# Optimization experiments

Hardware: AMD Instinct MI355X
Metric: run time of the kernel (lower is better)

Reference implementation:

```python
import jax, jax.numpy as jnp
import numpy as np

N = 8192   # number of points (p) == number of reference points (r); must match for final bmm
D = 1024   # feature width of the Linear projections


def setup_inputs() -> dict:
    key = jax.random.key(0)
    ks = jax.random.split(key, 8)
    s = 1.0 / np.sqrt(D)
    return {
        "p": jax.random.normal(ks[0], (N, D), dtype=jnp.float32),
        "r": jax.random.normal(ks[1], (N, D), dtype=jnp.float32),
        "Wh": jax.random.uniform(ks[2], (D, D), jnp.float32, -s, s),
        "bh": jax.random.uniform(ks[3], (D,), jnp.float32, -s, s),
        "Wl": jax.random.uniform(ks[4], (D, D), jnp.float32, -s, s),
        "bl": jax.random.uniform(ks[5], (D,), jnp.float32, -s, s),
        "Wg": jax.random.uniform(ks[6], (D, D), jnp.float32, -s, s),
        "bg": jax.random.uniform(ks[7], (D,), jnp.float32, -s, s),
    }


def reference(p, r, Wh, bh, Wl, bl, Wg, bg):
    # Linear projections (torch Linear: x @ W.T + b)
    q = p @ Wh.T + bh          # [N, D]  M_h(p)
    k = r @ Wl.T + bl          # [N, D]  M_l(r)
    v = p @ Wg.T + bg          # [N, D]  M_g(p)
    scores = q @ k.T           # [N, N]  == bmm(q[None], k[None].transpose(1,2))[0]
    # torch softmax dim=1 on [1, N, N] normalizes over the QUERY axis -> axis=0 here
    attn = jax.nn.softmax(scores, axis=0)
    return p + attn @ v        # residual add
```

## Files before the change

### kernel.cpp

```cpp
#include <hip/hip_runtime.h>
#include <hip/hip_fp16.h>

typedef _Float16 f16;
typedef __attribute__((ext_vector_type(8))) _Float16 f16x8;
typedef __attribute__((ext_vector_type(4))) float f32x4;

#define NPTS 8192
#define DIM  1024
#define HL2E 0.721347520444482f
#define S2SHIFT 50.0f
#define TBUF (128 * 32)

__device__ __forceinline__ void glds16(const void* g, void* l) {
  __builtin_amdgcn_global_load_lds(
      (const __attribute__((address_space(1))) void*)g,
      (__attribute__((address_space(3))) void*)l, 16, 0, 0);
}


__global__ void cvt_f32_f16(const float* __restrict__ src, f16* __restrict__ dst, int n) {
  int i = (blockIdx.x * 256 + threadIdx.x) * 8;
  if (i >= n) return;
  const float4* s = (const float4*)(src + i);
  float4 a = s[0], b = s[1];
  f16x8 o;
  o[0] = (f16)a.x; o[1] = (f16)a.y; o[2] = (f16)a.z; o[3] = (f16)a.w;
  o[4] = (f16)b.x; o[5] = (f16)b.y; o[6] = (f16)b.z; o[7] = (f16)b.w;
  *(f16x8*)(dst + i) = o;
}

__global__ void zero_f32(float* __restrict__ p, int n) {
  int i = blockIdx.x * 256 + threadIdx.x;
  if (i < n) p[i] = 0.f;
}

__global__ void mk_scales(const float* __restrict__ colsum,
                          f16* __restrict__ ics2, f16* __restrict__ ics4) {
  int j = blockIdx.x * 256 + threadIdx.x;
  float r2 = rsqrtf(colsum[j]);
  ics2[j] = (f16)r2;
  ics4[j] = (f16)sqrtf(r2);
}

__global__ void vscale(f16* __restrict__ vt, const f16* __restrict__ ics2) {
  long i = ((long)blockIdx.x * 256 + threadIdx.x) * 8;
  f16x8 v = *(f16x8*)(vt + i);
  f16x8 s = *(const f16x8*)(ics2 + (i & (NPTS - 1)));
  *(f16x8*)(vt + i) = v * s;
}

__global__ void reduce_out(const float* __restrict__ p,
                           const float* __restrict__ pa,
                           const float* __restrict__ pb,
                           float* __restrict__ out) {
  long i = ((long)blockIdx.x * 256 + threadIdx.x) * 4;
  float4 a = *(const float4*)(p + i);
  float4 b = *(const float4*)(pa + i);
  float4 c = *(const float4*)(pb + i);
  a.x += b.x + c.x; a.y += b.y + c.y; a.z += b.z + c.z; a.w += b.w + c.w;
  *(float4*)(out + i) = a;
}

__global__ __launch_bounds__(256, 2)
void proj_fused(const f16* __restrict__ p_h, const f16* __restrict__ r_h,
                const f16* __restrict__ Wh, const f16* __restrict__ Wl,
                const f16* __restrict__ Wg,
                const float* __restrict__ bh, const float* __restrict__ bl,
                const float* __restrict__ bg,
                f16* __restrict__ q_h, f16* __restrict__ k_h,
                f16* __restrict__ vt_h) {
  __shared__ f16 sA[2 * TBUF];
  __shared__ f16 sB[2 * TBUF];
  const int sub = blockIdx.x >> 9;
  const int bl_ = blockIdx.x & 511;
  const long bi = (long)(bl_ & 63) * 128;
  const long bj = (long)(bl_ >> 6) * 128;
  const f16* A = (sub == 1) ? r_h : p_h;
  const f16* B = (sub == 0) ? Wh : (sub == 1) ? Wl : Wg;
  const float* bias = (sub == 0) ? bh : (sub == 1) ? bl : bg;

  const int t = threadIdx.x;
  const int w = t >> 6, l = t & 63;
  const int wm = (w >> 1) * 64, wn = (w & 1) * 64;
  const int lr = l & 15;
  const int fbase = lr * 32 + (((l >> 4) ^ ((lr >> 1) & 3)) * 8);
  const int grow = w * 16 + (l >> 2);
  const int gcol = ((l & 3) ^ ((l >> 3) & 3)) * 8;
  const f16* gA = A + (bi + grow) * (long)DIM + gcol;
  const f16* gB = B + (bj + grow) * (long)DIM + gcol;
  const int lw0 = (w * 16) * 32, lw1 = (64 + w * 16) * 32;

  glds16(gA, sA + lw0);
  glds16(gA + 64l * DIM, sA + lw1);
  glds16(gB, sB + lw0);
  glds16(gB + 64l * DIM, sB + lw1);
  gA += 32; gB += 32;

  f32x4 acc[4][4] = {};
  const int nk = DIM / 32;
  for (int k = 0; k < nk; k++) {
    const int cur = (k & 1) * TBUF, nxt = TBUF - cur;
    __syncthreads();
    if (k + 1 < nk) {
      glds16(gA, sA + nxt + lw0);
      glds16(gA + 64l * DIM, sA + nxt + lw1);
      glds16(gB, sB + nxt + lw0);
      glds16(gB + 64l * DIM, sB + nxt + lw1);
      gA += 32; gB += 32;
    }
    f16x8 af[4], bf[4];
#pragma unroll
    for (int mt = 0; mt < 4; mt++)
      af[mt] = *(const f16x8*)(sA + cur + (wm + mt * 16) * 32 + fbase);
#pragma unroll
    for (int nt = 0; nt < 4; nt++)
      bf[nt] = *(const f16x8*)(sB + cur + (wn + nt * 16) * 32 + fbase);
#pragma unroll
    for (int mt = 0; mt < 4; mt++)
#pragma unroll
      for (int nt = 0; nt < 4; nt++)
        acc[mt][nt] = __builtin_amdgcn_mfma_f32_16x16x32_f16(af[mt], bf[nt], acc[mt][nt], 0, 0, 0);
  }

  const int rbase = (l >> 4) * 4;
  f16* C = (sub == 0) ? q_h : (sub == 1) ? k_h : vt_h;
#pragma unroll
  for (int nt = 0; nt < 4; nt++) {
    const long col = bj + wn + nt * 16 + lr;
    const float bb = bias[col];
#pragma unroll
    for (int mt = 0; mt < 4; mt++) {
      const long row0 = bi + wm + mt * 16 + rbase;
      if (sub < 2) {
#pragma unroll
        for (int g = 0; g < 4; g++)
          C[(row0 + g) * DIM + col] = (f16)(acc[mt][nt][g] + bb);
      } else {
        union { unsigned long long u; f16 h[4]; } pk;
#pragma unroll
        for (int g = 0; g < 4; g++) pk.h[g] = (f16)(acc[mt][nt][g] + bb);
        *(unsigned long long*)(C + col * (long)NPTS + row0) = pk.u;
      }
    }
  }
}

__global__ __launch_bounds__(512, 2)
void gemm_qk(const f16* __restrict__ A, const f16* __restrict__ B,
             f16* __restrict__ S, float* __restrict__ colsum) {
  __shared__ f16 smem[4 * 16384];
  const int b = blockIdx.x;
  const int sx = b & 7;
  const int j = b >> 3;
  const long bi = (long)(j >> 2) * 256;
  const long bj = (long)(sx * 4 + (j & 3)) * 256;

  const int t = threadIdx.x;
  const int w = t >> 6, l = t & 63;
  const int wm = (w >> 2) * 128, wn = (w & 3) * 64;
  const int lr = l & 15;
  const int fbase = lr * 32 + (((l >> 4) ^ ((lr >> 1) & 3)) * 8);
  const int sro = t >> 2;
  const int scol = ((t & 3) ^ ((t >> 3) & 3)) * 8;
  const f16* gAs = A + (bi + sro) * (long)DIM + scol;
  const f16* gBs = B + (bj + sro) * (long)DIM + scol;
  const int ldst = w * 512;

#pragma unroll
  for (int tl = 0; tl < 3; ++tl) {
    f16* d = smem + tl * 16384;
    glds16(gAs + tl * 32,              d + ldst);
    glds16(gAs + tl * 32 + 128l * DIM, d + 4096 + ldst);
    glds16(gBs + tl * 32,              d + 8192 + ldst);
    glds16(gBs + tl * 32 + 128l * DIM, d + 12288 + ldst);
  }
  asm volatile("s_waitcnt vmcnt(8)" ::: "memory");
  __builtin_amdgcn_s_barrier();
  asm volatile("" ::: "memory");

  f32x4 acc[8][4] = {};
#pragma unroll 4
  for (int kt = 0; kt < 32; ++kt) {
    const f16* sa = smem + (kt & 3) * 16384;
    f16* d = smem + ((kt + 3) & 3) * 16384;
    const int ks = (kt + 3 < 32) ? (kt + 3) : 31;
    const f16* as_ = gAs + ks * 32;
    const f16* bs_ = gBs + ks * 32;
    f16x8 af[4], bf[4];

#pragma unroll
    for (int mt = 0; mt < 4; ++mt)
      af[mt] = *(const f16x8*)(sa + (wm + mt * 16) * 32 + fbase);
#pragma unroll
    for (int nt = 0; nt < 4; ++nt)
      bf[nt] = *(const f16x8*)(sa + 8192 + (wn + nt * 16) * 32 + fbase);
    glds16(as_,              d + ldst);
    glds16(as_ + 128l * DIM, d + 4096 + ldst);
#pragma unroll
    for (int mt = 0; mt < 4; ++mt)
#pragma unroll
      for (int nt = 0; nt < 4; ++nt)
        acc[mt][nt] = __builtin_amdgcn_mfma_f32_16x16x32_f16(af[mt], bf[nt], acc[mt][nt], 0, 0, 0);

#pragma unroll
    for (int mt = 0; mt < 4; ++mt)
      af[mt] = *(const f16x8*)(sa + (wm + 64 + mt * 16) * 32 + fbase);
    glds16(bs_,              d + 8192 + ldst);
    glds16(bs_ + 128l * DIM, d + 12288 + ldst);
#pragma unroll
    for (int mt = 0; mt < 4; ++mt)
#pragma unroll
      for (int nt = 0; nt < 4; ++nt)
        acc[4 + mt][nt] = __builtin_amdgcn_mfma_f32_16x16x32_f16(af[mt], bf[nt], acc[4 + mt][nt], 0, 0, 0);

    asm volatile("s_waitcnt vmcnt(8)" ::: "memory");
    __builtin_amdgcn_s_barrier();
    asm volatile("" ::: "memory");
  }

  const int rbase = (l >> 4) * 4;
  float csum[4] = {0.f, 0.f, 0.f, 0.f};
#pragma unroll
  for (int mt = 0; mt < 8; ++mt) {
#pragma unroll
    for (int g = 0; g < 4; ++g) {
      const long row = bi + wm + mt * 16 + rbase + g;
      f16* Srow = S + row * NPTS + bj + wn + lr;
#pragma unroll
      for (int nt = 0; nt < 4; ++nt) {
        float e = exp2f((acc[mt][nt][g] - S2SHIFT) * HL2E);
        e = fminf(e, 240.f);
        f16 eh = (f16)e;
        Srow[nt * 16] = eh;
        float ef = (float)eh;
        csum[nt] += ef * ef;
      }
    }
  }
#pragma unroll
  for (int nt = 0; nt < 4; ++nt) {
    float cs = csum[nt];
    cs += __shfl_xor(cs, 16);
    cs += __shfl_xor(cs, 32);
    if (l < 16) atomicAdd(colsum + (bj + wn + nt * 16 + lr), cs);
  }
}

__global__ __launch_bounds__(256, 2)
void gemm_pv(const f16* __restrict__ Sm, const f16* __restrict__ vt,
             const f16* __restrict__ ics4,
             float* __restrict__ part0, float* __restrict__ part1) {
  __shared__ f16 sA[2 * TBUF];
  __shared__ f16 sB[2 * TBUF];
  const int split = blockIdx.x >> 9;
  const int bl_ = blockIdx.x & 511;
  const long bi = (long)(bl_ & 63) * 128;
  const long bj = (long)(bl_ >> 6) * 128;
  const long koff = (long)split * (NPTS / 2);

  const int t = threadIdx.x;
  const int w = t >> 6, l = t & 63;
  const int wm = (w >> 1) * 64, wn = (w & 1) * 64;
  const int lr = l & 15;
  const int fbase = lr * 32 + (((l >> 4) ^ ((lr >> 1) & 3)) * 8);
  const int grow = w * 16 + (l >> 2);
  const int gcol = ((l & 3) ^ ((l >> 3) & 3)) * 8;
  const f16* gB = vt + (bj + grow) * (long)NPTS + koff + gcol;
  const int lw0 = (w * 16) * 32, lw1 = (64 + w * 16) * 32;

  const int sr = t >> 2, sc = (t & 3) * 8;
  const int ssw = ((t & 3) ^ ((t >> 3) & 3)) * 8;
  const f16* gAs = Sm + (bi + sr) * (long)NPTS + koff + sc;
  const f16* gIc = ics4 + koff + sc;
  f16x8 ra0, ra1, icv;

  const int nk = (NPTS / 2) / 32;

  ra0 = *(const f16x8*)gAs;
  ra1 = *(const f16x8*)(gAs + 64l * NPTS);
  icv = *(const f16x8*)gIc;
  {
    f16x8 t0 = ra0 * icv; t0 = t0 * t0;
    f16x8 t1 = ra1 * icv; t1 = t1 * t1;
    *(f16x8*)(sA + sr * 32 + ssw) = t0;
    *(f16x8*)(sA + (sr + 64) * 32 + ssw) = t1;
  }
  gAs += 32; gIc += 32;
  ra0 = *(const f16x8*)gAs;
  ra1 = *(const f16x8*)(gAs + 64l * NPTS);
  icv = *(const f16x8*)gIc;
  glds16(gB, sB + lw0);
  glds16(gB + 64l * NPTS, sB + lw1);
  gB += 32;

  f32x4 acc[4][4] = {};
  for (int k = 0; k < nk; k++) {
    const int cur = (k & 1) * TBUF, nxt = TBUF - cur;
    __syncthreads();
    if (k + 1 < nk) {
      f16x8 t0 = ra0 * icv; t0 = t0 * t0;
      f16x8 t1 = ra1 * icv; t1 = t1 * t1;
      *(f16x8*)(sA + nxt + sr * 32 + ssw) = t0;
      *(f16x8*)(sA + nxt + (sr + 64) * 32 + ssw) = t1;
      if (k + 2 < nk) {
        gAs += 32; gIc += 32;
        ra0 = *(const f16x8*)gAs;
        ra1 = *(const f16x8*)(gAs + 64l * NPTS);
        icv = *(const f16x8*)gIc;
      }
      glds16(gB, sB + nxt + lw0);
      glds16(gB + 64l * NPTS, sB + nxt + lw1);
      gB += 32;
    }
    f16x8 af[4], bf[4];
#pragma unroll
    for (int mt = 0; mt < 4; mt++)
      af[mt] = *(const f16x8*)(sA + cur + (wm + mt * 16) * 32 + fbase);
#pragma unroll
    for (int nt = 0; nt < 4; nt++)
      bf[nt] = *(const f16x8*)(sB + cur + (wn + nt * 16) * 32 + fbase);
#pragma unroll
    for (int mt = 0; mt < 4; mt++)
#pragma unroll
      for (int nt = 0; nt < 4; nt++)
        acc[mt][nt] = __builtin_amdgcn_mfma_f32_16x16x32_f16(af[mt], bf[nt], acc[mt][nt], 0, 0, 0);
  }

  float* part = split ? part1 : part0;
  const int rbase = (l >> 4) * 4;
#pragma unroll
  for (int nt = 0; nt < 4; nt++) {
    const long col = bj + wn + nt * 16 + lr;
#pragma unroll
    for (int mt = 0; mt < 4; mt++) {
      const long row0 = bi + wm + mt * 16 + rbase;
#pragma unroll
      for (int g = 0; g < 4; g++)
        part[(row0 + g) * DIM + col] = acc[mt][nt][g];
    }
  }
}

extern "C" void kernel_launch(void* const* d_in, const int* in_sizes, int n_in,
                              void* d_out, int out_size, void* d_ws, size_t ws_size,
                              hipStream_t stream) {
  const float* p  = (const float*)d_in[0];
  const float* r  = (const float*)d_in[1];
  const float* Wh = (const float*)d_in[2];
  const float* bh = (const float*)d_in[3];
  const float* Wl = (const float*)d_in[4];
  const float* bl = (const float*)d_in[5];
  const float* Wg = (const float*)d_in[6];
  const float* bg = (const float*)d_in[7];
  float* out = (float*)d_out;

  char* ws = (char*)d_ws;
  f16* q_h  = (f16*)(ws + (0ull  << 20));
  f16* k_h  = (f16*)(ws + (16ull << 20));
  f16* vt_h = (f16*)(ws + (32ull << 20));
  f16* p_h  = (f16*)(ws + (48ull << 20));
  f16* r_h  = (f16*)(ws + (64ull << 20));
  f16* wh_h = (f16*)(ws + (80ull << 20));
  f16* wl_h = (f16*)(ws + (82ull << 20));
  f16* wg_h = (f16*)(ws + (84ull << 20));
  f16* S    = (f16*)(ws + (96ull << 20));
  float* colsum = (float*)(ws + (224ull << 20));
  f16* ics2 = (f16*)(ws + (225ull << 20));
  f16* ics4 = (f16*)(ws + (226ull << 20));
  float* part0 = (float*)(ws + (0ull  << 20));
  float* part1 = (float*)(ws + (48ull << 20));

  const int nP = NPTS * DIM, nW = DIM * DIM;
  cvt_f32_f16<<<nP / 2048, 256, 0, stream>>>(p,  p_h,  nP);
  cvt_f32_f16<<<nP / 2048, 256, 0, stream>>>(r,  r_h,  nP);
  cvt_f32_f16<<<nW / 2048, 256, 0, stream>>>(Wh, wh_h, nW);
  cvt_f32_f16<<<nW / 2048, 256, 0, stream>>>(Wl, wl_h, nW);
  cvt_f32_f16<<<nW / 2048, 256, 0, stream>>>(Wg, wg_h, nW);
  zero_f32<<<NPTS / 256, 256, 0, stream>>>(colsum, NPTS);

  dim3 blk(256);
  proj_fused<<<1536, blk, 0, stream>>>(p_h, r_h, wh_h, wl_h, wg_h,
                                       bh, bl, bg, q_h, k_h, vt_h);
  gemm_qk<<<1024, dim3(512), 0, stream>>>(q_h, k_h, S, colsum);
  mk_scales<<<NPTS / 256, 256, 0, stream>>>(colsum, ics2, ics4);
  vscale<<<(NPTS / 8) * (DIM / 256), 256, 0, stream>>>(vt_h, ics2);
  gemm_pv<<<1024, blk, 0, stream>>>(S, vt_h, ics4, part0, part1);
  reduce_out<<<nP / 1024, 256, 0, stream>>>(p, part0, part1, out);
}
```

Measured before the change: 537.7 us.

## Restructure PV GEMM with 256x256 tiles and 4-stage async LDS pipeline

Rewrites gemm_pv to use 512-thread blocks computing 256x256 output tiles. Both operands are now staged through global_load_lds into a 4-deep shared-memory ring with explicit vmcnt waits, replacing the register-staged, double-buffered A path. The per-column rescale and squaring of S is moved to after the LDS read. Block indices are remapped for cache locality, and colsum is clamped before rsqrt. This aims to raise data reuse and hide load latency, at the cost of higher register pressure (8x4 accumulators) and only 256 blocks, which is close to one per CU.

```diff
diff --git a/kernel.cpp b/kernel.cpp
--- a/kernel.cpp
+++ b/kernel.cpp
@@ -37,7 +37,7 @@
 __global__ void mk_scales(const float* __restrict__ colsum,
                           f16* __restrict__ ics2, f16* __restrict__ ics4) {
   int j = blockIdx.x * 256 + threadIdx.x;
-  float r2 = rsqrtf(colsum[j]);
+  float r2 = rsqrtf(fmaxf(colsum[j], 1e-20f));
   ics2[j] = (f16)r2;
   ics4[j] = (f16)sqrtf(r2);
 }
@@ -246,97 +246,111 @@
   }
 }
 
-__global__ __launch_bounds__(256, 2)
+__global__ __launch_bounds__(512, 2)
 void gemm_pv(const f16* __restrict__ Sm, const f16* __restrict__ vt,
              const f16* __restrict__ ics4,
              float* __restrict__ part0, float* __restrict__ part1) {
-  __shared__ f16 sA[2 * TBUF];
-  __shared__ f16 sB[2 * TBUF];
-  const int split = blockIdx.x >> 9;
-  const int bl_ = blockIdx.x & 511;
-  const long bi = (long)(bl_ & 63) * 128;
-  const long bj = (long)(bl_ >> 6) * 128;
+  __shared__ f16 smem[4 * 16384];
+  const int b = blockIdx.x;
+  const int sx = b & 7;
+  const int q = b >> 3;
+  const int bjidx = q & 3;
+  const int pr = (q >> 2) * 8 + sx;
+  const int split = pr >> 5;
+  const long bi = (long)(pr & 31) * 256;
+  const long bj = (long)bjidx * 256;
   const long koff = (long)split * (NPTS / 2);
 
   const int t = threadIdx.x;
   const int w = t >> 6, l = t & 63;
-  const int wm = (w >> 1) * 64, wn = (w & 1) * 64;
+  const int wm = (w >> 2) * 128, wn = (w & 3) * 64;
   const int lr = l & 15;
   const int fbase = lr * 32 + (((l >> 4) ^ ((lr >> 1) & 3)) * 8);
-  const int grow = w * 16 + (l >> 2);
-  const int gcol = ((l & 3) ^ ((l >> 3) & 3)) * 8;
-  const f16* gB = vt + (bj + grow) * (long)NPTS + koff + gcol;
-  const int lw0 = (w * 16) * 32, lw1 = (64 + w * 16) * 32;
-
-  const int sr = t >> 2, sc = (t & 3) * 8;
-  const int ssw = ((t & 3) ^ ((t >> 3) & 3)) * 8;
-  const f16* gAs = Sm + (bi + sr) * (long)NPTS + koff + sc;
-  const f16* gIc = ics4 + koff + sc;
-  f16x8 ra0, ra1, icv;
+  const int sro = t >> 2;
+  const int scol = ((t & 3) ^ ((t >> 3) & 3)) * 8;
+  const f16* gAs = Sm + (bi + sro) * (long)NPTS + koff + scol;
+  const f16* gBs = vt + (bj + sro) * (long)NPTS + koff + scol;
+  const f16* gic = ics4 + koff + (l >> 4) * 8;
+  const int ldst = w * 512;
 
   const int nk = (NPTS / 2) / 32;
 
-  ra0 = *(const f16x8*)gAs;
-  ra1 = *(const f16x8*)(gAs + 64l * NPTS);
-  icv = *(const f16x8*)gIc;
-  {
-    f16x8 t0 = ra0 * icv; t0 = t0 * t0;
-    f16x8 t1 = ra1 * icv; t1 = t1 * t1;
-    *(f16x8*)(sA + sr * 32 + ssw) = t0;
-    *(f16x8*)(sA + (sr + 64) * 32 + ssw) = t1;
-  }
-  gAs += 32; gIc += 32;
-  ra0 = *(const f16x8*)gAs;
-  ra1 = *(const f16x8*)(gAs + 64l * NPTS);
-  icv = *(const f16x8*)gIc;
-  glds16(gB, sB + lw0);
-  glds16(gB + 64l * NPTS, sB + lw1);
-  gB += 32;
-
-  f32x4 acc[4][4] = {};
-  for (int k = 0; k < nk; k++) {
-    const int cur = (k & 1) * TBUF, nxt = TBUF - cur;
-    __syncthreads();
-    if (k + 1 < nk) {
-      f16x8 t0 = ra0 * icv; t0 = t0 * t0;
-      f16x8 t1 = ra1 * icv; t1 = t1 * t1;
-      *(f16x8*)(sA + nxt + sr * 32 + ssw) = t0;
-      *(f16x8*)(sA + nxt + (sr + 64) * 32 + ssw) = t1;
-      if (k + 2 < nk) {
-        gAs += 32; gIc += 32;
-        ra0 = *(const f16x8*)gAs;
-        ra1 = *(const f16x8*)(gAs + 64l * NPTS);
-        icv = *(const f16x8*)gIc;
-      }
-      glds16(gB, sB + nxt + lw0);
-      glds16(gB + 64l * NPTS, sB + nxt + lw1);
-      gB += 32;
-    }
+  f16x8 icf[2];
+  icf[0] = *(const f16x8*)(gic);
+  icf[1] = *(const f16x8*)(gic + 32);
+#pragma unroll
+  for (int tl = 0; tl < 3; ++tl) {
+    f16* d = smem + tl * 16384;
+    glds16(gAs + tl * 32,               d + ldst);
+    glds16(gAs + tl * 32 + 128l * NPTS, d + 4096 + ldst);
+    glds16(gBs + tl * 32,               d + 8192 + ldst);
+    glds16(gBs + tl * 32 + 128l * NPTS, d + 12288 + ldst);
+  }
+  asm volatile("s_waitcnt vmcnt(8)" ::: "memory");
+  __builtin_amdgcn_s_barrier();
+  asm volatile("" ::: "memory");
+
+  f32x4 acc[8][4] = {};
+#pragma unroll 4
+  for (int kt = 0; kt < nk; ++kt) {
+    const f16* sa = smem + (kt & 3) * 16384;
+    f16* d = smem + ((kt + 3) & 3) * 16384;
+    const int ks = (kt + 3 < nk) ? (kt + 3) : nk - 1;
+    const int ki = (kt + 2 < nk) ? (kt + 2) : nk - 1;
+    const f16* as_ = gAs + ks * 32;
+    const f16* bs_ = gBs + ks * 32;
     f16x8 af[4], bf[4];
-#pragma unroll
-    for (int mt = 0; mt < 4; mt++)
-      af[mt] = *(const f16x8*)(sA + cur + (wm + mt * 16) * 32 + fbase);
-#pragma unroll
-    for (int nt = 0; nt < 4; nt++)
-      bf[nt] = *(const f16x8*)(sB + cur + (wn + nt * 16) * 32 + fbase);
-#pragma unroll
-    for (int mt = 0; mt < 4; mt++)
-#pragma unroll
-      for (int nt = 0; nt < 4; nt++)
+
+    const f16x8 ic_now = icf[kt & 1];
+    icf[kt & 1] = *(const f16x8*)(gic + ki * 32);
+
+#pragma unroll
+    for (int mt = 0; mt < 4; ++mt) {
+      af[mt] = *(const f16x8*)(sa + (wm + mt * 16) * 32 + fbase);
+      af[mt] = af[mt] * ic_now;
+      af[mt] = af[mt] * af[mt];
+    }
+#pragma unroll
+    for (int nt = 0; nt < 4; ++nt)
+      bf[nt] = *(const f16x8*)(sa + 8192 + (wn + nt * 16) * 32 + fbase);
+    glds16(as_,               d + ldst);
+    glds16(as_ + 128l * NPTS, d + 4096 + ldst);
+#pragma unroll
+    for (int mt = 0; mt < 4; ++mt)
+#pragma unroll
+      for (int nt = 0; nt < 4; ++nt)
         acc[mt][nt] = __builtin_amdgcn_mfma_f32_16x16x32_f16(af[mt], bf[nt], acc[mt][nt], 0, 0, 0);
+
+#pragma unroll
+    for (int mt = 0; mt < 4; ++mt) {
+      af[mt] = *(const f16x8*)(sa + (wm + 64 + mt * 16) * 32 + fbase);
+      af[mt] = af[mt] * ic_now;
+      af[mt] = af[mt] * af[mt];
+    }
+    glds16(bs_,               d + 8192 + ldst);
+    glds16(bs_ + 128l * NPTS, d + 12288 + ldst);
+#pragma unroll
+    for (int mt = 0; mt < 4; ++mt)
+#pragma unroll
+      for (int nt = 0; nt < 4; ++nt)
+        acc[4 + mt][nt] = __builtin_amdgcn_mfma_f32_16x16x32_f16(af[mt], bf[nt], acc[4 + mt][nt], 0, 0, 0);
+
+    asm volatile("s_waitcnt vmcnt(10)" ::: "memory");
+    __builtin_amdgcn_s_barrier();
+    asm volatile("" ::: "memory");
   }
 
   float* part = split ? part1 : part0;
   const int rbase = (l >> 4) * 4;
 #pragma unroll
-  for (int nt = 0; nt < 4; nt++) {
-    const long col = bj + wn + nt * 16 + lr;
-#pragma unroll
-    for (int mt = 0; mt < 4; mt++) {
-      const long row0 = bi + wm + mt * 16 + rbase;
-#pragma unroll
-      for (int g = 0; g < 4; g++)
-        part[(row0 + g) * DIM + col] = acc[mt][nt][g];
+  for (int mt = 0; mt < 8; ++mt) {
+#pragma unroll
+    for (int g = 0; g < 4; ++g) {
+      const long row = bi + wm + mt * 16 + rbase + g;
+      float* Prow = part + row * DIM + bj + wn + lr;
+#pragma unroll
+      for (int nt = 0; nt < 4; ++nt)
+        Prow[nt * 16] = acc[mt][nt][g];
     }
   }
 }
@@ -384,6 +398,6 @@
   gemm_qk<<<1024, dim3(512), 0, stream>>>(q_h, k_h, S, colsum);
   mk_scales<<<NPTS / 256, 256, 0, stream>>>(colsum, ics2, ics4);
   vscale<<<(NPTS / 8) * (DIM / 256), 256, 0, stream>>>(vt_h, ics2);
-  gemm_pv<<<1024, blk, 0, stream>>>(S, vt_h, ics4, part0, part1);
+  gemm_pv<<<256, dim3(512), 0, stream>>>(S, vt_h, ics4, part0, part1);
   reduce_out<<<nP / 1024, 256, 0, stream>>>(p, part0, part1, out);
 }
```

Measured after the change: 501.4 us. 1.07x faster.
